# Performance work log

Measured on AMD Instinct MI355X. Metric: run time of the kernel, lower is better.

## Reference

```python
import jax, jax.numpy as jnp
import numpy as np

# spikingjelly LIFNode defaults
TAU = 2.0
V_TH = 1.0
V_RESET = 0.0
ATAN_ALPHA = 2.0
LN_EPS = 1e-5


@jax.custom_vjp
def atan_spike(x):
    # Heaviside forward, ATan surrogate backward
    return (x >= 0).astype(x.dtype)

def _atan_fwd(x):
    return atan_spike(x), x

def _atan_bwd(x, g):
    sg = (ATAN_ALPHA / 2.0) / (1.0 + (jnp.pi / 2.0 * ATAN_ALPHA * x) ** 2)
    return (g * sg,)

atan_spike.defvjp(_atan_fwd, _atan_bwd)


def lif_multistep(x_seq):
    # x_seq: [T, B, D]; LIF with decay_input=True, hard reset, detach_reset=True
    def step(v, x):
        h = v + (x - (v - V_RESET)) / TAU          # charge
        s = atan_spike(h - V_TH)                    # fire
        s_d = jax.lax.stop_gradient(s)              # detach_reset
        v_next = h * (1.0 - s_d) + V_RESET * s_d    # hard reset
        return v_next, s
    v0 = jnp.zeros_like(x_seq[0])
    _, spikes = jax.lax.scan(step, v0, x_seq)
    return spikes


def layernorm(x, w, b):
    mu = jnp.mean(x, axis=-1, keepdims=True)
    var = jnp.mean((x - mu) ** 2, axis=-1, keepdims=True)
    return (x - mu) * jax.lax.rsqrt(var + LN_EPS) * w + b


def setup_inputs() -> dict:
    key = jax.random.key(0)
    k1, k2 = jax.random.split(key)
    T, B, D = 32, 128, 2048
    x_seq = jax.random.normal(k1, (T, B, D), dtype=jnp.float32)
    # Linear(dim, dim) kaiming-uniform-ish init
    lim = 1.0 / np.sqrt(D)
    W = jax.random.uniform(k2, (D, D), minval=-lim, maxval=lim, dtype=jnp.float32)
    b = jnp.zeros((D,), dtype=jnp.float32)
    ln_w = jnp.ones((D,), dtype=jnp.float32)
    ln_b = jnp.zeros((D,), dtype=jnp.float32)
    return {"x_seq": x_seq, "W": W, "b": b, "ln_w": ln_w, "ln_b": ln_b}


def reference(x_seq, W, b, ln_w, ln_b):
    identity = x_seq
    out = jnp.einsum('tbd,ed->tbe', x_seq, W) + b   # Linear(dim, dim)
    out = layernorm(out, ln_w, ln_b)
    return lif_multistep(out + identity)
```

## Files before the change

kernel.cpp:

```cpp
#include <hip/hip_runtime.h>
#include <math.h>

constexpr int T_ = 32, B_ = 128, D_ = 2048;
constexpr int M_ = T_ * B_;
constexpr double LN_EPS = 1e-5;

constexpr size_t YD_BYTES = (size_t)M_ * D_ * sizeof(double);
constexpr size_t ST_BYTES = (size_t)M_ * 2 * sizeof(double);

#if defined(__has_builtin)
#if __has_builtin(__builtin_amdgcn_mfma_f64_16x16x4f64)
#define HAVE_MFMA_F64 1
#endif
#endif
#ifndef HAVE_MFMA_F64
#define HAVE_MFMA_F64 0
#endif

#if HAVE_MFMA_F64
typedef double d4 __attribute__((ext_vector_type(4)));
constexpr int BM = 128, BN = 128, BK = 32;

template <int MODE>
__global__ __launch_bounds__(256, 2) void gemm_k(
    const float* __restrict__ X, const float* __restrict__ W,
    const float* __restrict__ bias, double* __restrict__ Yd,
    float* __restrict__ Yf)
{
    __shared__ float As[BK][BM + 4];
    __shared__ float Bs[BK][BN + 4];

    const int wid = blockIdx.x;
    const int swz = (wid & 7) * 64 + (wid >> 3);
    const int bx  = swz >> 5;
    const int by  = swz & 31;
    const int m0 = by * BM, n0 = bx * BN;
    const int tid = threadIdx.x;

    const int sr = tid >> 1;
    const int sc = (tid & 1) << 4;
    const float* xg = X + (size_t)(m0 + sr) * D_ + sc;
    const float* wg = W + (size_t)(n0 + sr) * D_ + sc;

    const int lane = tid & 63;
    const int wv   = tid >> 6;
    const int wr   = (wv >> 1) * 64;
    const int wc   = (wv & 1) * 64;
    const int li   = lane & 15;
    const int lk   = lane >> 4;

    d4 p1 = __builtin_amdgcn_mfma_f64_16x16x4f64((double)li, 1.0, (d4)0.0, 0, 0, 0);
    d4 p2 = __builtin_amdgcn_mfma_f64_16x16x4f64(1.0, (double)li, (d4)0.0, 0, 0, 0);
    int ri[4], cj[4];
#pragma unroll
    for (int v = 0; v < 4; ++v) {
        ri[v] = (int)(p1[v] * 0.25 + 0.5);
        cj[v] = (int)(p2[v] * 0.25 + 0.5);
    }

    d4 acc[4][4];
#pragma unroll
    for (int mt = 0; mt < 4; ++mt)
#pragma unroll
        for (int nt = 0; nt < 4; ++nt) acc[mt][nt] = (d4)0.0;

    for (int k0 = 0; k0 < D_; k0 += BK) {
        float4 xa[4], wb[4];
#pragma unroll
        for (int j = 0; j < 4; ++j) {
            xa[j] = *(const float4*)(xg + k0 + 4 * j);
            wb[j] = *(const float4*)(wg + k0 + 4 * j);
        }
        __syncthreads();
#pragma unroll
        for (int j = 0; j < 4; ++j)
#pragma unroll
            for (int e = 0; e < 4; ++e) {
                As[sc + 4 * j + e][sr] = ((const float*)&xa[j])[e];
                Bs[sc + 4 * j + e][sr] = ((const float*)&wb[j])[e];
            }
        __syncthreads();
#pragma unroll
        for (int s = 0; s < BK / 4; ++s) {
            const int k = 4 * s + lk;
            double a[4], b[4];
#pragma unroll
            for (int mt = 0; mt < 4; ++mt)
                a[mt] = (double)As[k][wr + mt * 16 + li];
#pragma unroll
            for (int nt = 0; nt < 4; ++nt)
                b[nt] = (double)Bs[k][wc + nt * 16 + li];
#pragma unroll
            for (int mt = 0; mt < 4; ++mt)
#pragma unroll
                for (int nt = 0; nt < 4; ++nt)
                    acc[mt][nt] = __builtin_amdgcn_mfma_f64_16x16x4f64(
                        a[mt], b[nt], acc[mt][nt], 0, 0, 0);
        }
    }

#pragma unroll
    for (int nt = 0; nt < 4; ++nt) {
#pragma unroll
        for (int mt = 0; mt < 4; ++mt) {
#pragma unroll
            for (int v = 0; v < 4; ++v) {
                const int row = m0 + wr + mt * 16 + ri[v];
                const int col = n0 + wc + nt * 16 + cj[v];
                const double val = acc[mt][nt][v] + (double)bias[col];
                if (MODE == 0) Yd[(size_t)row * D_ + col] = val;
                else           Yf[(size_t)row * D_ + col] = (float)val;
            }
        }
    }
}

#else
constexpr int BM = 128, BN = 128, BK = 16;

template <int MODE>
__global__ __launch_bounds__(256, 2) void gemm_k(
    const float* __restrict__ X, const float* __restrict__ W,
    const float* __restrict__ bias, double* __restrict__ Yd,
    float* __restrict__ Yf)
{
    __shared__ float As[BK][BM + 4];
    __shared__ float Bs[BK][BN + 4];
    const int wid = blockIdx.x;
    const int swz = (wid & 7) * 64 + (wid >> 3);
    const int bx  = swz >> 5;
    const int by  = swz & 31;
    const int m0 = by * BM, n0 = bx * BN;
    const int tid = threadIdx.x;
    const int lr = tid >> 2;
    const int lc = (tid & 3) << 2;
    const float* xg = X + (size_t)(m0 + lr) * D_ + lc;
    const float* wg = W + (size_t)(n0 + lr) * D_ + lc;
    const int tx = tid & 15;
    const int ty = tid >> 4;

    double acc[8][8];
#pragma unroll
    for (int i = 0; i < 8; ++i)
#pragma unroll
        for (int j = 0; j < 8; ++j) acc[i][j] = 0.0;

    for (int k0 = 0; k0 < D_; k0 += BK) {
        float4 a0 = *(const float4*)(xg + k0);
        float4 a1 = *(const float4*)(xg + (size_t)64 * D_ + k0);
        float4 b0 = *(const float4*)(wg + k0);
        float4 b1 = *(const float4*)(wg + (size_t)64 * D_ + k0);
        __syncthreads();
        As[lc + 0][lr] = a0.x; As[lc + 1][lr] = a0.y;
        As[lc + 2][lr] = a0.z; As[lc + 3][lr] = a0.w;
        As[lc + 0][64 + lr] = a1.x; As[lc + 1][64 + lr] = a1.y;
        As[lc + 2][64 + lr] = a1.z; As[lc + 3][64 + lr] = a1.w;
        Bs[lc + 0][lr] = b0.x; Bs[lc + 1][lr] = b0.y;
        Bs[lc + 2][lr] = b0.z; Bs[lc + 3][lr] = b0.w;
        Bs[lc + 0][64 + lr] = b1.x; Bs[lc + 1][64 + lr] = b1.y;
        Bs[lc + 2][64 + lr] = b1.z; Bs[lc + 3][64 + lr] = b1.w;
        __syncthreads();
#pragma unroll
        for (int k = 0; k < BK; ++k) {
            float af[8], bf[8];
            *(float4*)&af[0] = *(const float4*)&As[k][ty * 4];
            *(float4*)&af[4] = *(const float4*)&As[k][64 + ty * 4];
            *(float4*)&bf[0] = *(const float4*)&Bs[k][tx * 4];
            *(float4*)&bf[4] = *(const float4*)&Bs[k][64 + tx * 4];
            double ad[8], bd[8];
#pragma unroll
            for (int i = 0; i < 8; ++i) { ad[i] = (double)af[i]; bd[i] = (double)bf[i]; }
#pragma unroll
            for (int i = 0; i < 8; ++i)
#pragma unroll
                for (int j = 0; j < 8; ++j)
                    acc[i][j] = fma(ad[i], bd[j], acc[i][j]);
        }
    }
#pragma unroll
    for (int jh = 0; jh < 2; ++jh) {
        const int col = n0 + jh * 64 + tx * 4;
        const float4 bb4 = *(const float4*)&bias[col];
        const double bb[4] = {(double)bb4.x, (double)bb4.y,
                              (double)bb4.z, (double)bb4.w};
#pragma unroll
        for (int ih = 0; ih < 2; ++ih)
#pragma unroll
            for (int i = 0; i < 4; ++i) {
                const int r = m0 + ih * 64 + ty * 4 + i;
#pragma unroll
                for (int v = 0; v < 4; ++v) {
                    const double val = acc[ih * 4 + i][jh * 4 + v] + bb[v];
                    if (MODE == 0) Yd[(size_t)r * D_ + col + v] = val;
                    else           Yf[(size_t)r * D_ + col + v] = (float)val;
                }
            }
    }
}
#endif

template <bool SRC64>
__global__ __launch_bounds__(256) void ln_stats_k(
    const void* __restrict__ Ysrc, double* __restrict__ stats)
{
    __shared__ double red[8];
    const int row = blockIdx.x;
    const int tid = threadIdx.x;
    double a[8];
    if constexpr (SRC64) {
        const double2* y = (const double2*)((const double*)Ysrc + (size_t)row * D_);
        double2 u0 = y[tid], u1 = y[tid + 256], u2 = y[tid + 512], u3 = y[tid + 768];
        a[0] = u0.x; a[1] = u0.y; a[2] = u1.x; a[3] = u1.y;
        a[4] = u2.x; a[5] = u2.y; a[6] = u3.x; a[7] = u3.y;
    } else {
        const float4* y = (const float4*)((const float*)Ysrc + (size_t)row * D_);
        float4 u0 = y[tid], u1 = y[tid + 256];
        a[0] = u0.x; a[1] = u0.y; a[2] = u0.z; a[3] = u0.w;
        a[4] = u1.x; a[5] = u1.y; a[6] = u1.z; a[7] = u1.w;
    }

    double s = 0.0;
#pragma unroll
    for (int i = 0; i < 8; ++i) s += a[i];
#pragma unroll
    for (int off = 32; off > 0; off >>= 1) s += __shfl_xor(s, off);
    const int lane = tid & 63, wv = tid >> 6;
    if (lane == 0) red[wv] = s;
    __syncthreads();
    const double mean = (red[0] + red[1] + red[2] + red[3]) * (1.0 / D_);

    double d2 = 0.0;
#pragma unroll
    for (int i = 0; i < 8; ++i) { double d = a[i] - mean; d2 += d * d; }
#pragma unroll
    for (int off = 32; off > 0; off >>= 1) d2 += __shfl_xor(d2, off);
    if (lane == 0) red[4 + wv] = d2;
    __syncthreads();
    if (tid == 0) {
        const double var = (red[4] + red[5] + red[6] + red[7]) * (1.0 / D_);
        stats[2 * row]     = mean;
        stats[2 * row + 1] = 1.0 / sqrt(var + LN_EPS);
    }
}

template <bool SRC64>
__global__ __launch_bounds__(256) void lif_k(
    const float* __restrict__ X, const float* __restrict__ lnw,
    const float* __restrict__ lnb, const double* __restrict__ stats,
    const void* __restrict__ Ysrc, float* __restrict__ out)
{
    const int q  = blockIdx.x * blockDim.x + threadIdx.x;
    const int e4 = q & (D_ / 4 - 1);
    const int bi = q >> 9;

    const float4 w4 = ((const float4*)lnw)[e4];
    const float4 b4 = ((const float4*)lnb)[e4];
    const double w[4]  = {(double)w4.x, (double)w4.y, (double)w4.z, (double)w4.w};
    const double bb[4] = {(double)b4.x, (double)b4.y, (double)b4.z, (double)b4.w};
    double v[4] = {0.0, 0.0, 0.0, 0.0};

    for (int t = 0; t < T_; ++t) {
        const int row = t * B_ + bi;
        const double mu = stats[2 * row];
        const double rs = stats[2 * row + 1];
        double y[4];
        if constexpr (SRC64) {
            const double2* yp = (const double2*)((const double*)Ysrc +
                                                 (size_t)row * D_ + e4 * 4);
            double2 u0 = yp[0], u1 = yp[1];
            y[0] = u0.x; y[1] = u0.y; y[2] = u1.x; y[3] = u1.y;
        } else {
            float4 y4 = ((const float4*)Ysrc)[(size_t)row * (D_ / 4) + e4];
            y[0] = y4.x; y[1] = y4.y; y[2] = y4.z; y[3] = y4.w;
        }
        const float4 x4 = ((const float4*)X)[(size_t)row * (D_ / 4) + e4];
        const double xr[4] = {(double)x4.x, (double)x4.y, (double)x4.z, (double)x4.w};
        float sp[4];
#pragma unroll
        for (int c = 0; c < 4; ++c) {
            const double z   = (y[c] - mu) * rs * w[c] + bb[c];
            const double xin = z + xr[c];
            const double h   = v[c] + (xin - v[c]) * 0.5;
            const bool fire  = (h - 1.0) >= 0.0;
            sp[c] = fire ? 1.0f : 0.0f;
            v[c]  = fire ? 0.0 : h;
        }
        float4 o = {sp[0], sp[1], sp[2], sp[3]};
        ((float4*)out)[(size_t)row * (D_ / 4) + e4] = o;
    }
}

extern "C" void kernel_launch(void* const* d_in, const int* in_sizes, int n_in,
                              void* d_out, int out_size, void* d_ws, size_t ws_size,
                              hipStream_t stream)
{
    const float* X    = (const float*)d_in[0];
    const float* W    = (const float*)d_in[1];
    const float* bias = (const float*)d_in[2];
    const float* lnw  = (const float*)d_in[3];
    const float* lnb  = (const float*)d_in[4];
    float* out = (float*)d_out;

    const bool big = ws_size >= YD_BYTES + ST_BYTES;

    if (big) {
        double* Yd    = (double*)d_ws;
        double* stats = (double*)((char*)d_ws + YD_BYTES);
        gemm_k<0><<<dim3(512), dim3(256), 0, stream>>>(X, W, bias, Yd, nullptr);
        ln_stats_k<true><<<dim3(M_), dim3(256), 0, stream>>>(Yd, stats);
        lif_k<true><<<dim3((B_ * D_ / 4) / 256), dim3(256), 0, stream>>>(
            X, lnw, lnb, stats, Yd, out);
    } else {
        double* stats = (double*)d_ws;
        gemm_k<1><<<dim3(512), dim3(256), 0, stream>>>(X, W, bias, nullptr, out);
        ln_stats_k<false><<<dim3(M_), dim3(256), 0, stream>>>(out, stats);
        lif_k<false><<<dim3((B_ * D_ / 4) / 256), dim3(256), 0, stream>>>(
            X, lnw, lnb, stats, out, out);
    }
}
```

Measured before the change: 558.0 us.

## Double-buffer LDS tiles and prefetch next K-slice in FP64 MFMA GEMM

```diff
diff --git a/kernel.cpp b/kernel.cpp
--- a/kernel.cpp
+++ b/kernel.cpp
@@ -20,6 +20,7 @@
 #if HAVE_MFMA_F64
 typedef double d4 __attribute__((ext_vector_type(4)));
 constexpr int BM = 128, BN = 128, BK = 32;
+constexpr int LDP = BM + 16;
 
 template <int MODE>
 __global__ __launch_bounds__(256, 2) void gemm_k(
@@ -27,8 +28,8 @@
     const float* __restrict__ bias, double* __restrict__ Yd,
     float* __restrict__ Yf)
 {
-    __shared__ float As[BK][BM + 4];
-    __shared__ float Bs[BK][BN + 4];
+    __shared__ float As[2][BK][LDP];
+    __shared__ float Bs[2][BK][LDP];
 
     const int wid = blockIdx.x;
     const int swz = (wid & 7) * 64 + (wid >> 3);
@@ -64,38 +65,60 @@
 #pragma unroll
         for (int nt = 0; nt < 4; ++nt) acc[mt][nt] = (d4)0.0;
 
+    float4 xa[4], wb[4];
+
+#pragma unroll
+    for (int j = 0; j < 4; ++j) {
+        xa[j] = *(const float4*)(xg + 4 * j);
+        wb[j] = *(const float4*)(wg + 4 * j);
+    }
+#pragma unroll
+    for (int j = 0; j < 4; ++j)
+#pragma unroll
+        for (int e = 0; e < 4; ++e) {
+            As[0][sc + 4 * j + e][sr] = ((const float*)&xa[j])[e];
+            Bs[0][sc + 4 * j + e][sr] = ((const float*)&wb[j])[e];
+        }
+    __syncthreads();
+
+    int cur = 0;
     for (int k0 = 0; k0 < D_; k0 += BK) {
-        float4 xa[4], wb[4];
-#pragma unroll
-        for (int j = 0; j < 4; ++j) {
-            xa[j] = *(const float4*)(xg + k0 + 4 * j);
-            wb[j] = *(const float4*)(wg + k0 + 4 * j);
-        }
-        __syncthreads();
-#pragma unroll
-        for (int j = 0; j < 4; ++j)
-#pragma unroll
-            for (int e = 0; e < 4; ++e) {
-                As[sc + 4 * j + e][sr] = ((const float*)&xa[j])[e];
-                Bs[sc + 4 * j + e][sr] = ((const float*)&wb[j])[e];
+        const bool has_next = (k0 + BK < D_);
+        if (has_next) {
+#pragma unroll
+            for (int j = 0; j < 4; ++j) {
+                xa[j] = *(const float4*)(xg + k0 + BK + 4 * j);
+                wb[j] = *(const float4*)(wg + k0 + BK + 4 * j);
             }
-        __syncthreads();
+        }
 #pragma unroll
         for (int s = 0; s < BK / 4; ++s) {
             const int k = 4 * s + lk;
             double a[4], b[4];
 #pragma unroll
             for (int mt = 0; mt < 4; ++mt)
-                a[mt] = (double)As[k][wr + mt * 16 + li];
+                a[mt] = (double)As[cur][k][wr + mt * 16 + li];
 #pragma unroll
             for (int nt = 0; nt < 4; ++nt)
-                b[nt] = (double)Bs[k][wc + nt * 16 + li];
+                b[nt] = (double)Bs[cur][k][wc + nt * 16 + li];
 #pragma unroll
             for (int mt = 0; mt < 4; ++mt)
 #pragma unroll
                 for (int nt = 0; nt < 4; ++nt)
                     acc[mt][nt] = __builtin_amdgcn_mfma_f64_16x16x4f64(
                         a[mt], b[nt], acc[mt][nt], 0, 0, 0);
+        }
+        if (has_next) {
+            const int nxt = cur ^ 1;
+#pragma unroll
+            for (int j = 0; j < 4; ++j)
+#pragma unroll
+                for (int e = 0; e < 4; ++e) {
+                    As[nxt][sc + 4 * j + e][sr] = ((const float*)&xa[j])[e];
+                    Bs[nxt][sc + 4 * j + e][sr] = ((const float*)&wb[j])[e];
+                }
+            __syncthreads();
+            cur = nxt;
         }
     }
 
```

Result: no change. 549.8 us (median of 2 runs) (-1.5%).
